# Performance work log

Hardware: AMD Instinct MI355X
Metric: run time of the kernel (lower is better)

## Reference

```python
import jax, jax.numpy as jnp
import numpy as np

FD, FO, FK, H = 1024, 512, 128, 4
N = 32768


def setup_inputs() -> dict:
    key = jax.random.key(0)
    ks = jax.random.split(key, 8)
    s = 0.02
    return {
        "Xd": jax.random.normal(ks[0], (N, FD), dtype=jnp.float32),
        "Xo": jax.random.normal(ks[1], (N, FO), dtype=jnp.float32),
        "Wq": jax.random.normal(ks[2], (FO, FK * H), dtype=jnp.float32) * s,
        "bq": jnp.zeros((FK * H,), dtype=jnp.float32),
        "Wk": jax.random.normal(ks[3], (FD, FK * H), dtype=jnp.float32) * s,
        "bk": jnp.zeros((FK * H,), dtype=jnp.float32),
        "Wv": jax.random.normal(ks[4], (FD, FD * H), dtype=jnp.float32) * s,
        "bv": jnp.zeros((FD * H,), dtype=jnp.float32),
    }


def reference(Xd, Xo, Wq, bq, Wk, bk, Wv, bv):
    n = Xd.shape[0]
    Q = (Xo @ Wq + bq).reshape(n, H, FK)      # (n, H, fk)
    K = (Xd @ Wk + bk).reshape(n, H, FK)      # (n, H, fk)
    V = (Xd @ Wv + bv).reshape(n, H, FD)      # (n, H, fd)
    scores = jnp.sum(Q * K, axis=2, keepdims=True)  # (n, H, 1), no softmax
    Z = scores * V                              # (n, H, fd)
    Z = jnp.max(Z, axis=1)                      # max pooling over heads -> (n, fd)
    return Z  # dropout is identity in inference
```

## Files before the change

### kernel.cpp

```cpp
#include <hip/hip_runtime.h>

typedef __attribute__((ext_vector_type(8))) short short8;
typedef __attribute__((ext_vector_type(4))) float f32x4;

#define GLL16(gp, lp) __builtin_amdgcn_global_load_lds( \
    (__attribute__((address_space(1))) void*)(gp), \
    (__attribute__((address_space(3))) void*)(lp), 16, 0, 0)

__device__ __forceinline__ unsigned short f2b(float f) {
  unsigned int u = __builtin_bit_cast(unsigned int, f);
  u += 0x7fffu + ((u >> 16) & 1u);
  return (unsigned short)(u >> 16);
}
__device__ __forceinline__ float b2f(unsigned short s) {
  unsigned int u = ((unsigned int)s) << 16;
  return __builtin_bit_cast(float, u);
}

__global__ __launch_bounds__(256) void conv_k(const float* __restrict__ in,
                                              short8* __restrict__ out, long n8) {
  for (long i = (long)blockIdx.x * 256 + threadIdx.x; i < n8;
       i += (long)gridDim.x * 256) {
    const float4* p = (const float4*)in + 2 * i;
    float4 a = p[0], b = p[1];
    short8 v;
    v[0] = (short)f2b(a.x); v[1] = (short)f2b(a.y);
    v[2] = (short)f2b(a.z); v[3] = (short)f2b(a.w);
    v[4] = (short)f2b(b.x); v[5] = (short)f2b(b.y);
    v[6] = (short)f2b(b.z); v[7] = (short)f2b(b.w);
    out[i] = v;
  }
}

__global__ __launch_bounds__(256) void tconv_k(const float* __restrict__ in,
                                               unsigned short* __restrict__ out,
                                               int K, int C, int inter) {
  __shared__ float t[32][33];
  int k0 = blockIdx.x * 32, c0 = blockIdx.y * 32;
  int tx = threadIdx.x & 31, ty = threadIdx.x >> 5;
#pragma unroll
  for (int p = 0; p < 4; ++p)
    t[ty + p * 8][tx] = in[(size_t)(k0 + ty + p * 8) * C + c0 + tx];
  __syncthreads();
#pragma unroll
  for (int p = 0; p < 4; ++p) {
    int c = ty + p * 8;
    int gc = c0 + c;
    int orow = inter ? ((gc & 1023) * 4 + (gc >> 10)) : gc;
    out[(size_t)orow * K + k0 + tx] = f2b(t[tx][c]);
  }
}

template <int KD>
__global__ __launch_bounds__(512, 4) void gemm_v2(
    const unsigned short* __restrict__ A, const unsigned short* __restrict__ Bt,
    const float* __restrict__ bias, const float* __restrict__ sc,
    float* __restrict__ Z) {
  __shared__ __align__(16) char lds[73728];
  __shared__ float s_sc[1024];

  constexpr int NKT = KD / 32;
  int tid = threadIdx.x;
  int bid = blockIdx.x;
  int cpx = gridDim.x >> 3;
  int lb = (bid & 7) * cpx + (bid >> 3);
  int mtile = lb >> 5, nt0 = lb & 31;
  long m0 = (long)mtile * 256;
  int l = tid & 63, wid = tid >> 6, wm = wid >> 1, wn = wid & 1;

  int srg = tid >> 3, slot = tid & 7;
  int se = slot ^ (srg & 7);
  int par = se >> 2, kc = se & 3;
  int rowb = srg * 2 + par;
  const char* aT = (const char*)(A + m0 * KD) + (long)rowb * (KD * 2) + kc * 16;
  const char* bT = (const char*)(Bt + (long)nt0 * 128 * KD) + (long)rowb * (KD * 2) + kc * 16;
  char* ldsb = (char*)lds;
  int dstOff = wid * 1024;

  auto stage = [&](int kt, int bb) {
    int ko = kt * 64;
    GLL16(aT + ko,                  ldsb + bb * 24576 + dstOff);
    GLL16(aT + 128 * (KD * 2) + ko, ldsb + bb * 24576 + 8192 + dstOff);
    GLL16(bT + ko,                  ldsb + bb * 24576 + 16384 + dstOff);
  };

  for (int i = tid; i < 1024; i += 512) s_sc[i] = sc[m0 * 4 + i];

  int ar = l & 15, kcl = l >> 4;
  int aoffR[4], boffR[4];
#pragma unroll
  for (int m = 0; m < 4; ++m) {
    int wr = wm * 64 + m * 16 + ar, sr = wr >> 1;
    aoffR[m] = sr * 128 + (((((wr & 1) << 2) | kcl) ^ (sr & 7)) << 4);
  }
#pragma unroll
  for (int n = 0; n < 4; ++n) {
    int br = wn * 64 + n * 16 + ar, sr = br >> 1;
    boffR[n] = 16384 + sr * 128 + (((((br & 1) << 2) | kcl) ^ (sr & 7)) << 4);
  }

  f32x4 zero = {0.f, 0.f, 0.f, 0.f};
  f32x4 acc[4][4];
#pragma unroll
  for (int m = 0; m < 4; ++m)
#pragma unroll
    for (int n = 0; n < 4; ++n) acc[m][n] = zero;

  stage(0, 0);
  stage(1, 1);

  for (int t = 0; t < NKT; ++t) {
    if (t + 1 < NKT) asm volatile("s_waitcnt vmcnt(3)" ::: "memory");
    else             asm volatile("s_waitcnt vmcnt(0)" ::: "memory");
    __builtin_amdgcn_s_barrier();
    asm volatile("" ::: "memory");
    if (t + 2 < NKT) stage(t + 2, (t + 2) % 3);

    const char* base = ldsb + (t % 3) * 24576;
    short8 af[4], bf[4];
#pragma unroll
    for (int m = 0; m < 4; ++m) af[m] = *(const short8*)(base + aoffR[m]);
#pragma unroll
    for (int n = 0; n < 4; ++n) bf[n] = *(const short8*)(base + boffR[n]);
#pragma unroll
    for (int m = 0; m < 4; ++m)
#pragma unroll
      for (int n = 0; n < 4; ++n)
        acc[m][n] = __builtin_amdgcn_mfma_f32_16x16x32_bf16(af[m], bf[n],
                                                            acc[m][n], 0, 0, 0);
  }

  __syncthreads();
  float* Zs = (float*)ldsb;
#pragma unroll
  for (int n = 0; n < 4; ++n) {
    int pl = wn * 64 + n * 16 + (l & 15);
    int pg = nt0 * 128 + pl;
    int h = pl & 3;
    float bb = bias[(pg & 3) * 1024 + (pg >> 2)];
#pragma unroll
    for (int m = 0; m < 4; ++m) {
      int rl = wm * 64 + m * 16 + ((l >> 4) << 2);
#pragma unroll
      for (int r = 0; r < 4; ++r) {
        float z = s_sc[(rl + r) * 4 + h] * (acc[m][n][r] + bb);
        z = fmaxf(z, __shfl_xor(z, 1));
        z = fmaxf(z, __shfl_xor(z, 2));
        if ((l & 3) == 0) Zs[(rl + r) * 32 + (pl >> 2)] = z;
      }
    }
  }
  __syncthreads();
#pragma unroll
  for (int it = 0; it < 4; ++it) {
    int i = it * 512 + tid;
    int row = i >> 3, q = i & 7;
    f32x4 v = *(const f32x4*)&Zs[row * 32 + q * 4];
    *(f32x4*)&Z[(m0 + row) * 1024 + nt0 * 32 + q * 4] = v;
  }
}

template <int KD, int NTI, int EPI>
__global__ __launch_bounds__(512, 2) void gemm_p(
    const unsigned short* __restrict__ A, const unsigned short* __restrict__ Bt,
    const float* __restrict__ bias, const unsigned short* __restrict__ Qb,
    unsigned short* __restrict__ outb, float* __restrict__ sc) {
  __shared__ __align__(16) char lds[131072];

  constexpr int NKT = KD / 64;
  int tid = threadIdx.x;
  int bid = blockIdx.x;
  int cpx = gridDim.x >> 3;
  int lb = (bid & 7) * cpx + (bid >> 3);
  int mtile = lb / NTI, nt0 = lb % NTI;
  long m0 = (long)mtile * 256;
  int l = tid & 63, wid = tid >> 6, wm = wid >> 2, wn = wid & 3;

  int rowg = tid >> 3;
  int swz = (tid & 7) ^ (rowg & 7);
  const char* aSrc = (const char*)(A + m0 * KD) + (long)rowg * (KD * 2) + swz * 16;
  const char* bSrc = (const char*)(Bt + (long)nt0 * 256 * KD) + (long)rowg * (KD * 2) + swz * 16;
  char* ldsb = (char*)lds;
  int dstOff = wid * 1024;

  auto stageA = [&](int hh, int tt) {
    char* base = ldsb + ((tt & 1) * 32768 + hh * 16384) + dstOff;
    const char* s = aSrc + (long)(hh * 128) * (KD * 2) + tt * 128;
    GLL16(s, base);
    GLL16(s + (long)64 * (KD * 2), base + 8192);
  };
  auto stageB = [&](int hh, int tt) {
    char* base = ldsb + 65536 + ((tt & 1) * 32768 + hh * 16384) + dstOff;
    const char* s = bSrc + (long)(hh * 128) * (KD * 2) + tt * 128;
    GLL16(s, base);
    GLL16(s + (long)64 * (KD * 2), base + 8192);
  };

  int ar = l & 15, kcl = l >> 4;
  int x0 = ((kcl ^ (ar & 7)) << 4);
  int x1 = (((4 | kcl) ^ (ar & 7)) << 4);
  int thrA = (wm * 64 + ar) * 128;
  int thrB = (wn * 32 + ar) * 128;

  short8 aA[4][2], aB[4][2], b0[2][2], b1[2][2];

#define RD_A(dst, slotoff)                                                  \
  do {                                                                      \
    const char* p_ = ldsb + (slotoff) + thrA;                               \
    _Pragma("unroll") for (int m_ = 0; m_ < 4; ++m_) {                      \
      dst[m_][0] = *(const short8*)(p_ + x0 + m_ * 2048);                   \
      dst[m_][1] = *(const short8*)(p_ + x1 + m_ * 2048);                   \
    }                                                                       \
  } while (0)
#define RD_B(dst, slotoff)                                                  \
  do {                                                                      \
    const char* p_ = ldsb + 65536 + (slotoff) + thrB;                       \
    _Pragma("unroll") for (int n_ = 0; n_ < 2; ++n_) {                      \
      dst[n_][0] = *(const short8*)(p_ + x0 + n_ * 2048);                   \
      dst[n_][1] = *(const short8*)(p_ + x1 + n_ * 2048);                   \
    }                                                                       \
  } while (0)
#define MFQ(q, am, bn)                                                      \
  do {                                                                      \
    __builtin_amdgcn_s_setprio(1);                                          \
    _Pragma("unroll") for (int m_ = 0; m_ < 4; ++m_)                        \
        _Pragma("unroll") for (int n_ = 0; n_ < 2; ++n_)                    \
            _Pragma("unroll") for (int k_ = 0; k_ < 2; ++k_)                \
                acc[q][m_ * 2 + n_] = __builtin_amdgcn_mfma_f32_16x16x32_bf16( \
                    am[m_][k_], bn[n_][k_], acc[q][m_ * 2 + n_], 0, 0, 0);  \
    __builtin_amdgcn_s_setprio(0);                                          \
  } while (0)
#define VM(n) asm volatile("s_waitcnt vmcnt(" #n ")" ::: "memory")
#define BAR() __builtin_amdgcn_s_barrier()
#define CLOB() asm volatile("" ::: "memory")

  f32x4 zero = {0.f, 0.f, 0.f, 0.f};
  f32x4 acc[4][8];
#pragma unroll
  for (int q = 0; q < 4; ++q)
#pragma unroll
    for (int f = 0; f < 8; ++f) acc[q][f] = zero;

  stageA(0, 0); stageB(0, 0); stageB(1, 0); stageA(1, 0);
  VM(4); BAR(); CLOB();
  RD_A(aA, 0);
  RD_B(b0, 0);

  for (int t = 0; t < NKT - 1; ++t) {
    int aS = (t & 1) * 32768;
    int bS = aS;
    int aS2 = aS ^ 32768;
    stageA(0, t + 1);
    VM(4); BAR(); CLOB();
    RD_B(b1, bS + 16384);
    MFQ(0, aA, b0);
    stageB(0, t + 1);
    VM(4); BAR(); CLOB();
    RD_A(aB, aS + 16384);
    MFQ(1, aA, b1);
    stageB(1, t + 1);
    VM(4); BAR(); CLOB();
    RD_A(aA, aS2);
    MFQ(2, aB, b0);
    stageA(1, t + 1);
    VM(4); BAR(); CLOB();
    RD_B(b0, aS2);
    MFQ(3, aB, b1);
  }
  {
    constexpr int t = NKT - 1;
    int aS = (t & 1) * 32768;
    VM(2); BAR(); CLOB();
    RD_B(b1, aS + 16384);
    MFQ(0, aA, b0);
    VM(0); BAR(); CLOB();
    RD_A(aB, aS + 16384);
    MFQ(1, aA, b1);
    MFQ(2, aB, b0);
    MFQ(3, aB, b1);
  }
#undef RD_A
#undef RD_B
#undef MFQ
#undef VM
#undef BAR
#undef CLOB

  if constexpr (EPI == 0) {
#pragma unroll
    for (int qm = 0; qm < 2; ++qm)
#pragma unroll
      for (int qn = 0; qn < 2; ++qn) {
        int q = qm * 2 + qn;
#pragma unroll
        for (int n = 0; n < 2; ++n) {
          int col = nt0 * 256 + qn * 128 + wn * 32 + n * 16 + (l & 15);
          float bb = bias[col];
#pragma unroll
          for (int m = 0; m < 4; ++m) {
            long rowb = m0 + qm * 128 + wm * 64 + m * 16 + ((l >> 4) << 2);
#pragma unroll
            for (int r = 0; r < 4; ++r)
              outb[(rowb + r) * 512 + col] = f2b(acc[q][m * 2 + n][r] + bb);
          }
        }
      }
  } else {
    float part[2][2][4][4];
#pragma unroll
    for (int qm = 0; qm < 2; ++qm)
#pragma unroll
      for (int qn = 0; qn < 2; ++qn)
#pragma unroll
        for (int m = 0; m < 4; ++m)
#pragma unroll
          for (int r = 0; r < 4; ++r) part[qm][qn][m][r] = 0.f;
#pragma unroll
    for (int qm = 0; qm < 2; ++qm)
#pragma unroll
      for (int qn = 0; qn < 2; ++qn) {
        int q = qm * 2 + qn;
#pragma unroll
        for (int n = 0; n < 2; ++n) {
          int col = nt0 * 256 + qn * 128 + wn * 32 + n * 16 + (l & 15);
          float bb = bias[col];
#pragma unroll
          for (int m = 0; m < 4; ++m) {
            long rowb = m0 + qm * 128 + wm * 64 + m * 16 + ((l >> 4) << 2);
#pragma unroll
            for (int r = 0; r < 4; ++r) {
              float kv = acc[q][m * 2 + n][r] + bb;
              part[qm][qn][m][r] += kv * b2f(Qb[(rowb + r) * 512 + col]);
            }
          }
        }
      }
    __syncthreads();
    float (*sred)[2][4] = (float(*)[2][4])ldsb;
#pragma unroll
    for (int qm = 0; qm < 2; ++qm)
#pragma unroll
      for (int qn = 0; qn < 2; ++qn)
#pragma unroll
        for (int m = 0; m < 4; ++m)
#pragma unroll
          for (int r = 0; r < 4; ++r) {
            float s = part[qm][qn][m][r];
            s += __shfl_xor(s, 1);
            s += __shfl_xor(s, 2);
            s += __shfl_xor(s, 4);
            s += __shfl_xor(s, 8);
            if ((l & 15) == 0)
              sred[qm * 128 + wm * 64 + m * 16 + ((l >> 4) << 2) + r][qn][wn] = s;
          }
    __syncthreads();
    {
      int row = tid >> 1, hh = tid & 1;
      float v = sred[row][hh][0] + sred[row][hh][1] + sred[row][hh][2] +
                sred[row][hh][3];
      sc[(m0 + row) * 4 + nt0 * 2 + hh] = v;
    }
  }
}

__global__ __launch_bounds__(256) void naive_k(
    const float* __restrict__ Xd, const float* __restrict__ Xo,
    const float* __restrict__ Wq, const float* __restrict__ bq,
    const float* __restrict__ Wk, const float* __restrict__ bk,
    const float* __restrict__ Wv, const float* __restrict__ bv,
    float* __restrict__ Z) {
  int i = blockIdx.x, t = threadIdx.x;
  __shared__ float xd[1024], xo[512], s[4];
  for (int j = t; j < 1024; j += 256) xd[j] = Xd[(size_t)i * 1024 + j];
  for (int j = t; j < 512; j += 256) xo[j] = Xo[(size_t)i * 512 + j];
  if (t < 4) s[t] = 0.f;
  __syncthreads();
  for (int c = t; c < 512; c += 256) {
    float q = bq[c], k = bk[c];
    for (int j = 0; j < 512; ++j) q += xo[j] * Wq[(size_t)j * 512 + c];
    for (int j = 0; j < 1024; ++j) k += xd[j] * Wk[(size_t)j * 512 + c];
    atomicAdd(&s[c >> 7], q * k);
  }
  __syncthreads();
  for (int d = t; d < 1024; d += 256) {
    float z = -INFINITY;
    for (int h = 0; h < 4; ++h) {
      float v = bv[h * 1024 + d];
      for (int j = 0; j < 1024; ++j) v += xd[j] * Wv[(size_t)j * 4096 + h * 1024 + d];
      z = fmaxf(z, s[h] * v);
    }
    Z[(size_t)i * 1024 + d] = z;
  }
}

extern "C" void kernel_launch(void* const* d_in, const int* in_sizes, int n_in,
                              void* d_out, int out_size, void* d_ws, size_t ws_size,
                              hipStream_t stream) {
  const float* Xd = (const float*)d_in[0];
  const float* Xo = (const float*)d_in[1];
  const float* Wq = (const float*)d_in[2];
  const float* bq = (const float*)d_in[3];
  const float* Wk = (const float*)d_in[4];
  const float* bk = (const float*)d_in[5];
  const float* Wv = (const float*)d_in[6];
  const float* bv = (const float*)d_in[7];
  float* Z = (float*)d_out;
  long N = in_sizes[0] / 1024;

  size_t sz_Xd = (size_t)N * 1024 * 2, sz_Xo = (size_t)N * 512 * 2;
  size_t sz_Wq = (size_t)512 * 512 * 2, sz_Wk = (size_t)512 * 1024 * 2;
  size_t sz_Wv = (size_t)4096 * 1024 * 2;
  size_t sz_Qb = (size_t)N * 512 * 2, sz_sc = (size_t)N * 4 * 4;
  size_t o_Xo = sz_Xd, o_Wq = o_Xo + sz_Xo, o_Wk = o_Wq + sz_Wq,
         o_Wv = o_Wk + sz_Wk, o_Qb = o_Wv + sz_Wv, o_sc = o_Qb + sz_Qb;
  size_t need = o_sc + sz_sc;

  if (ws_size < need || (N % 256) != 0) {
    naive_k<<<(int)N, 256, 0, stream>>>(Xd, Xo, Wq, bq, Wk, bk, Wv, bv, Z);
    return;
  }

  char* w = (char*)d_ws;
  unsigned short* Xd_b = (unsigned short*)w;
  unsigned short* Xo_b = (unsigned short*)(w + o_Xo);
  unsigned short* Wq_t = (unsigned short*)(w + o_Wq);
  unsigned short* Wk_t = (unsigned short*)(w + o_Wk);
  unsigned short* Wv_p = (unsigned short*)(w + o_Wv);
  unsigned short* Qb   = (unsigned short*)(w + o_Qb);
  float* sc = (float*)(w + o_sc);

  conv_k<<<2048, 256, 0, stream>>>(Xd, (short8*)Xd_b, N * 1024 / 8);
  conv_k<<<2048, 256, 0, stream>>>(Xo, (short8*)Xo_b, N * 512 / 8);
  tconv_k<<<dim3(16, 16), 256, 0, stream>>>(Wq, Wq_t, 512, 512, 0);
  tconv_k<<<dim3(32, 16), 256, 0, stream>>>(Wk, Wk_t, 1024, 512, 0);
  tconv_k<<<dim3(32, 128), 256, 0, stream>>>(Wv, Wv_p, 1024, 4096, 1);

  int mt = (int)(N / 256);
  gemm_p<512, 2, 0><<<mt * 2, 512, 0, stream>>>(Xo_b, Wq_t, bq, nullptr, Qb,
                                                nullptr);
  gemm_p<1024, 2, 1><<<mt * 2, 512, 0, stream>>>(Xd_b, Wk_t, bk, Qb, nullptr,
                                                 sc);
  gemm_v2<1024><<<mt * 32, 512, 0, stream>>>(Xd_b, Wv_p, bv, sc, Z);
}
```

Before: 472.1 us.

## Make V GEMM persistent: 256 blocks each loop over a panel of M tiles

Result: slower. 657.2 us (+39.2%).

```diff
diff --git a/kernel.cpp b/kernel.cpp
--- a/kernel.cpp
+++ b/kernel.cpp
@@ -52,39 +52,41 @@
 }
 
 template <int KD>
-__global__ __launch_bounds__(512, 4) void gemm_v2(
+__global__ __launch_bounds__(512, 2) void gemm_vper(
     const unsigned short* __restrict__ A, const unsigned short* __restrict__ Bt,
     const float* __restrict__ bias, const float* __restrict__ sc,
-    float* __restrict__ Z) {
-  __shared__ __align__(16) char lds[73728];
-  __shared__ float s_sc[1024];
+    float* __restrict__ Z, int PM) {
+  __shared__ __align__(16) char ring[73728];
+  __shared__ __align__(16) float Zs[256 * 32];
 
   constexpr int NKT = KD / 32;
+  constexpr long PANEL = 256L * KD * 2;
   int tid = threadIdx.x;
   int bid = blockIdx.x;
   int cpx = gridDim.x >> 3;
   int lb = (bid & 7) * cpx + (bid >> 3);
-  int mtile = lb >> 5, nt0 = lb & 31;
-  long m0 = (long)mtile * 256;
+  int nt0 = lb >> 3;
+  int mg = lb & 7;
+  long mrow0 = (long)mg * PM * 256;
   int l = tid & 63, wid = tid >> 6, wm = wid >> 1, wn = wid & 1;
 
   int srg = tid >> 3, slot = tid & 7;
   int se = slot ^ (srg & 7);
   int par = se >> 2, kc = se & 3;
   int rowb = srg * 2 + par;
-  const char* aT = (const char*)(A + m0 * KD) + (long)rowb * (KD * 2) + kc * 16;
+  const char* aT = (const char*)(A + mrow0 * KD) + (long)rowb * (KD * 2) + kc * 16;
   const char* bT = (const char*)(Bt + (long)nt0 * 128 * KD) + (long)rowb * (KD * 2) + kc * 16;
-  char* ldsb = (char*)lds;
+  char* ldsb = (char*)ring;
   int dstOff = wid * 1024;
 
-  auto stage = [&](int kt, int bb) {
-    int ko = kt * 64;
-    GLL16(aT + ko,                  ldsb + bb * 24576 + dstOff);
-    GLL16(aT + 128 * (KD * 2) + ko, ldsb + bb * 24576 + 8192 + dstOff);
-    GLL16(bT + ko,                  ldsb + bb * 24576 + 16384 + dstOff);
+  const int TOT = PM * NKT;
+  auto stage = [&](int g) {
+    long ko = (long)(g >> 5) * PANEL + (g & 31) * 64;
+    int bb = (g % 3) * 24576;
+    GLL16(aT + ko,                  ldsb + bb + dstOff);
+    GLL16(aT + 128 * (KD * 2) + ko, ldsb + bb + 8192 + dstOff);
+    GLL16(bT + (g & 31) * 64,       ldsb + bb + 16384 + dstOff);
   };
-
-  for (int i = tid; i < 1024; i += 512) s_sc[i] = sc[m0 * 4 + i];
 
   int ar = l & 15, kcl = l >> 4;
   int aoffR[4], boffR[4];
@@ -106,17 +108,17 @@
 #pragma unroll
     for (int n = 0; n < 4; ++n) acc[m][n] = zero;
 
-  stage(0, 0);
-  stage(1, 1);
-
-  for (int t = 0; t < NKT; ++t) {
-    if (t + 1 < NKT) asm volatile("s_waitcnt vmcnt(3)" ::: "memory");
+  stage(0);
+  stage(1);
+
+  for (int g = 0; g < TOT; ++g) {
+    if (g + 1 < TOT) asm volatile("s_waitcnt vmcnt(3)" ::: "memory");
     else             asm volatile("s_waitcnt vmcnt(0)" ::: "memory");
     __builtin_amdgcn_s_barrier();
     asm volatile("" ::: "memory");
-    if (t + 2 < NKT) stage(t + 2, (t + 2) % 3);
-
-    const char* base = ldsb + (t % 3) * 24576;
+    if (g + 2 < TOT) stage(g + 2);
+
+    const char* base = ldsb + (g % 3) * 24576;
     short8 af[4], bf[4];
 #pragma unroll
     for (int m = 0; m < 4; ++m) af[m] = *(const short8*)(base + aoffR[m]);
@@ -128,35 +130,47 @@
       for (int n = 0; n < 4; ++n)
         acc[m][n] = __builtin_amdgcn_mfma_f32_16x16x32_bf16(af[m], bf[n],
                                                             acc[m][n], 0, 0, 0);
-  }
-
-  __syncthreads();
-  float* Zs = (float*)ldsb;
-#pragma unroll
-  for (int n = 0; n < 4; ++n) {
-    int pl = wn * 64 + n * 16 + (l & 15);
-    int pg = nt0 * 128 + pl;
-    int h = pl & 3;
-    float bb = bias[(pg & 3) * 1024 + (pg >> 2)];
-#pragma unroll
-    for (int m = 0; m < 4; ++m) {
-      int rl = wm * 64 + m * 16 + ((l >> 4) << 2);
-#pragma unroll
-      for (int r = 0; r < 4; ++r) {
-        float z = s_sc[(rl + r) * 4 + h] * (acc[m][n][r] + bb);
-        z = fmaxf(z, __shfl_xor(z, 1));
-        z = fmaxf(z, __shfl_xor(z, 2));
-        if ((l & 3) == 0) Zs[(rl + r) * 32 + (pl >> 2)] = z;
+
+    if ((g & 31) == 31) {
+      long m0 = mrow0 + (long)(g >> 5) * 256;
+      float scv[4][4];
+#pragma unroll
+      for (int m = 0; m < 4; ++m)
+#pragma unroll
+        for (int r = 0; r < 4; ++r)
+          scv[m][r] = sc[(m0 + wm * 64 + m * 16 + ((l >> 4) << 2) + r) * 4 + (l & 3)];
+#pragma unroll
+      for (int n = 0; n < 4; ++n) {
+        int pl = wn * 64 + n * 16 + (l & 15);
+        int pg = nt0 * 128 + pl;
+        float bb = bias[(pg & 3) * 1024 + (pg >> 2)];
+#pragma unroll
+        for (int m = 0; m < 4; ++m) {
+          int rl = wm * 64 + m * 16 + ((l >> 4) << 2);
+#pragma unroll
+          for (int r = 0; r < 4; ++r) {
+            float z = scv[m][r] * (acc[m][n][r] + bb);
+            z = fmaxf(z, __shfl_xor(z, 1));
+            z = fmaxf(z, __shfl_xor(z, 2));
+            if ((l & 3) == 0) Zs[(rl + r) * 32 + (pl >> 2)] = z;
+          }
+        }
       }
+      asm volatile("s_waitcnt lgkmcnt(0)" ::: "memory");
+      __builtin_amdgcn_s_barrier();
+      asm volatile("" ::: "memory");
+#pragma unroll
+      for (int it = 0; it < 4; ++it) {
+        int i = it * 512 + tid;
+        int row = i >> 3, q = i & 7;
+        f32x4 v = *(const f32x4*)&Zs[row * 32 + q * 4];
+        *(f32x4*)&Z[(m0 + row) * 1024 + nt0 * 32 + q * 4] = v;
+      }
+#pragma unroll
+      for (int m = 0; m < 4; ++m)
+#pragma unroll
+        for (int n = 0; n < 4; ++n) acc[m][n] = zero;
     }
-  }
-  __syncthreads();
-#pragma unroll
-  for (int it = 0; it < 4; ++it) {
-    int i = it * 512 + tid;
-    int row = i >> 3, q = i & 7;
-    f32x4 v = *(const f32x4*)&Zs[row * 32 + q * 4];
-    *(f32x4*)&Z[(m0 + row) * 1024 + nt0 * 32 + q * 4] = v;
   }
 }
 
@@ -415,7 +429,8 @@
          o_Wv = o_Wk + sz_Wk, o_Qb = o_Wv + sz_Wv, o_sc = o_Qb + sz_Qb;
   size_t need = o_sc + sz_sc;
 
-  if (ws_size < need || (N % 256) != 0) {
+  long mtiles = N / 256;
+  if (ws_size < need || (N % 256) != 0 || (mtiles % 8) != 0) {
     naive_k<<<(int)N, 256, 0, stream>>>(Xd, Xo, Wq, bq, Wk, bk, Wv, bv, Z);
     return;
   }
@@ -435,10 +450,11 @@
   tconv_k<<<dim3(32, 16), 256, 0, stream>>>(Wk, Wk_t, 1024, 512, 0);
   tconv_k<<<dim3(32, 128), 256, 0, stream>>>(Wv, Wv_p, 1024, 4096, 1);
 
-  int mt = (int)(N / 256);
+  int mt = (int)mtiles;
+  int PM = mt / 8;
   gemm_p<512, 2, 0><<<mt * 2, 512, 0, stream>>>(Xo_b, Wq_t, bq, nullptr, Qb,
                                                 nullptr);
   gemm_p<1024, 2, 1><<<mt * 2, 512, 0, stream>>>(Xd_b, Wk_t, bk, Qb, nullptr,
                                                  sc);
-  gemm_v2<1024><<<mt * 32, 512, 0, stream>>>(Xd_b, Wv_p, bv, sc, Z);
-}
+  gemm_vper<1024><<<256, 512, 0, stream>>>(Xd_b, Wv_p, bv, sc, Z, PM);
+}
```
